# Kernel optimization log

Measured on AMD Instinct MI355X. Metric: run time of the kernel, lower is better.

Reference implementation:

```python
import jax, jax.numpy as jnp
import numpy as np

K = 8  # kNN fan-in (includes self at distance 0, matching torch_cluster.knn)


def _mlp2(x, w1, b1, w2, b2):
    # PyG MLP with plain_last=True: act between layers, none after last
    h = jax.nn.relu(x @ w1 + b1)
    return h @ w2 + b2


def _dynamic_edge_conv(x, w1, b1, w2, b2, k=K):
    # x: [B, N, C]. Recompute kNN graph from current features, EdgeConv with
    # message = MLP([x_i, x_j - x_i]) and max aggregation over neighbors.
    sq = jnp.sum(x * x, axis=-1)                                   # [B, N]
    d2 = sq[:, :, None] + sq[:, None, :] - 2.0 * jnp.einsum('bnc,bmc->bnm', x, x)
    _, idx = jax.lax.top_k(-d2, k)                                 # [B, N, k]
    xj = jax.vmap(lambda xx, ii: xx[ii])(x, idx)                   # [B, N, k, C]
    xi = jnp.broadcast_to(x[:, :, None, :], xj.shape)
    e = jnp.concatenate([xi, xj - xi], axis=-1)                    # [B, N, k, 2C]
    msg = _mlp2(e, w1, b1, w2, b2)                                 # [B, N, k, C_out]
    return jnp.max(msg, axis=2)                                    # [B, N, C_out]


def setup_inputs() -> dict:
    key = jax.random.key(0)
    ks = jax.random.split(key, 24)
    B, N = 2, 1000
    S = 0.05
    p = lambda i, shape: jax.random.normal(ks[i], shape, jnp.float32) * S
    return dict(
        pos=jax.random.normal(ks[0], (B, N, 3), jnp.float32),
        c1_w1=p(1, (6, 16)),   c1_b1=p(2, (16,)),  c1_w2=p(3, (16, 32)),   c1_b2=p(4, (32,)),
        c2_w1=p(5, (64, 64)),  c2_b1=p(6, (64,)),  c2_w2=p(7, (64, 128)),  c2_b2=p(8, (128,)),
        c3_w1=p(9, (256, 256)), c3_b1=p(10, (256,)), c3_w2=p(11, (256, 512)), c3_b2=p(12, (512,)),
        sm_w1=p(13, (672, 256)), sm_b1=p(14, (256,)), sm_w2=p(15, (256, 128)), sm_b2=p(16, (128,)),
        ec_w1=p(17, (384, 128)), ec_b1=p(18, (128,)), ec_w2=p(19, (128, 1)), ec_b2=p(20, (1,)),
    )


def reference(pos, c1_w1, c1_b1, c1_w2, c1_b2, c2_w1, c2_b1, c2_w2, c2_b2,
              c3_w1, c3_b1, c3_w2, c3_b2, sm_w1, sm_b1, sm_w2, sm_b2,
              ec_w1, ec_b1, ec_w2, ec_b2):
    x1 = _dynamic_edge_conv(pos, c1_w1, c1_b1, c1_w2, c1_b2)       # [B, N, 32]
    x2 = _dynamic_edge_conv(x1, c2_w1, c2_b1, c2_w2, c2_b2)        # [B, N, 128]
    x3 = _dynamic_edge_conv(x2, c3_w1, c3_b1, c3_w2, c3_b2)        # [B, N, 512]
    x = jnp.concatenate([x1, x2, x3], axis=-1)                     # [B, N, 672]
    sf = _mlp2(x, sm_w1, sm_b1, sm_w2, sm_b2)                      # [B, N, 128]
    g = jnp.max(sf, axis=1)                                        # [B, 128] global max pool

    N = pos.shape[1]
    t0, t1 = np.triu_indices(N, 1)                                 # 499500 pairs
    D = sf.shape[-1]
    # Linear(cat[feat_i, feat_j, global]) split into three small GEMMs on
    # [B,N,128] / [B,128] then gathered to pairs: identical math, avoids the
    # [B, P, 384] concat the torch code materializes.
    hi = sf @ ec_w1[:D]                                            # [B, N, 128]
    hj = sf @ ec_w1[D:2 * D]                                       # [B, N, 128]
    hg = g @ ec_w1[2 * D:] + ec_b1                                 # [B, 128]
    hidden = jax.nn.relu(hi[:, t0] + hj[:, t1] + hg[:, None, :])   # [B, P, 128]
    mlp_out = (hidden @ ec_w2 + ec_b2)[..., 0]                     # [B, P]
    pair_prob = jax.nn.sigmoid(mlp_out)
    return pair_prob, mlp_out
```

## Files before the change

### kernel.cpp

```cpp
#include <hip/hip_runtime.h>
#include <hip/hip_bf16.h>
#include <cmath>

#define NB 2
#define NP 1000
#define KNN 8
#define PPAIR 499500
#define JSPLIT 8

typedef __hip_bfloat16 bf16;
typedef unsigned long long u64;
typedef unsigned short ushort;
typedef unsigned int uint;
typedef __attribute__((ext_vector_type(8))) short short8;
typedef __attribute__((ext_vector_type(4))) float f32x4;

__device__ __forceinline__ float b2f(bf16 v) { return __bfloat162float(v); }
__device__ __forceinline__ ushort f2b(float f) {
    uint x = __float_as_uint(f);
    return (ushort)((x + 0x7FFFu + ((x >> 16) & 1u)) >> 16);
}
__device__ __forceinline__ float ldin(const void* p, int flag, int i) {
    return flag ? ((const float*)p)[i] : b2f(((const bf16*)p)[i]);
}

#define OFF_POS    0
#define OFF_C1W1   6000
#define OFF_C1B1   6096
#define OFF_C1W2   6112
#define OFF_C1B2   6624
#define OFF_C2W1   6656
#define OFF_C2B1   10752
#define OFF_C2W2   10816
#define OFF_C2B2   19008
#define OFF_C3W1   19136
#define OFF_C3B1   84672
#define OFF_C3W2   84928
#define OFF_C3B2   216000
#define OFF_SMW1   216512
#define OFF_SMB1   388544
#define OFF_SMW2   388800
#define OFF_SMB2   421568
#define OFF_ECW1   421696
#define OFF_ECB1   470848
#define OFF_ECW2   470976
#define OFF_ECB2   471104
#define OFF_X1     471112
#define OFF_X2     535112
#define OFF_X3     791112
#define OFF_SF     1815112
#define OFF_G      2071112
#define OFF_HI     2071368
#define OFF_HJ     2327368
#define OFF_HG     2583368
#define OFF_FLAG   2583624
#define OFF_NIDX   2583632
#define OFF_GP     2599632
#define OFF_W1T    2606032
#define OFF_W2T    2638800
#define OFF_SMW1T  2704336
#define OFF_SMW2T  2790352
#define OFF_ECW1T  2806736
#define OFF_PL     2823120
#define OFF_E2W1T  3079120
#define OFF_E2W2T  3081168

__global__ void detect_kernel(const void* pos, int* flag) {
    __shared__ float red[256];
    const unsigned short* p = (const unsigned short*)pos;
    float m = 0.f;
    for (int t = threadIdx.x; t < 6000; t += 256) {
        unsigned int u = ((unsigned int)p[t]) << 16;
        float v = fabsf(__uint_as_float(u));
        if (!isfinite(v)) v = 1e30f;
        m = fmaxf(m, v);
    }
    red[threadIdx.x] = m;
    __syncthreads();
    for (int s = 128; s > 0; s >>= 1) {
        if (threadIdx.x < s) red[threadIdx.x] = fmaxf(red[threadIdx.x], red[threadIdx.x + s]);
        __syncthreads();
    }
    if (threadIdx.x == 0) flag[0] = (red[0] > 1e6f) ? 1 : 0;
}

struct InPtrs { const void* p[21]; };

__global__ void cvt_all_kernel(InPtrs in, float* ws, const int* flag,
                               ushort* w1t, ushort* w2t, ushort* smw1t,
                               ushort* smw2t, ushort* ecw1t,
                               ushort* e2w1t, ushort* e2w2t) {
    const int sizes[21] = {6000, 96, 16, 512, 32, 4096, 64, 8192, 128,
                           65536, 256, 131072, 512, 172032, 256, 32768, 128,
                           49152, 128, 128, 1};
    const int offs[21] = {OFF_POS, OFF_C1W1, OFF_C1B1, OFF_C1W2, OFF_C1B2,
                          OFF_C2W1, OFF_C2B1, OFF_C2W2, OFF_C2B2,
                          OFF_C3W1, OFF_C3B1, OFF_C3W2, OFF_C3B2,
                          OFF_SMW1, OFF_SMB1, OFF_SMW2, OFF_SMB2,
                          OFF_ECW1, OFF_ECB1, OFF_ECW2, OFF_ECB2};
    int y = blockIdx.y;
    int t = blockIdx.x * 256 + threadIdx.x;
    int f = flag[0];
    if (y < 21) {
        if (t < sizes[y]) ws[offs[y] + t] = ldin(in.p[y], f, t);
    } else if (y == 21) {
        if (t < 65536) {
            int h = t >> 8, c = t & 255;
            w1t[t] = f2b(ldin(in.p[9], f, c * 256 + h));
        }
    } else if (y == 22) {
        if (t < 131072) {
            int o = t >> 8, h = t & 255;
            w2t[t] = f2b(ldin(in.p[11], f, h * 512 + o));
        }
    } else if (y == 23) {
        if (t < 172032) {
            int h = t / 672, c = t - h * 672;
            smw1t[t] = f2b(ldin(in.p[13], f, c * 256 + h));
        }
    } else if (y == 24) {
        if (t < 32768) {
            int o = t >> 8, h = t & 255;
            smw2t[t] = f2b(ldin(in.p[15], f, h * 128 + o));
        }
    } else if (y == 25) {
        if (t < 32768) {
            int op = t >> 7, c = t & 127;
            int idx = (op < 128) ? (c * 128 + op) : ((128 + c) * 128 + (op - 128));
            ecw1t[t] = f2b(ldin(in.p[17], f, idx));
        }
    } else if (y == 26) {
        if (t < 4096) {
            int h = t >> 6, c = t & 63;
            e2w1t[t] = f2b(ldin(in.p[5], f, c * 64 + h));
        }
    } else {
        if (t < 8192) {
            int o = t >> 6, h = t & 63;
            e2w2t[t] = f2b(ldin(in.p[7], f, h * 128 + o));
        }
    }
}

__device__ __forceinline__ void ce(u64& a, u64& b) {
    u64 lo = a < b ? a : b;
    u64 hi = a < b ? b : a;
    a = lo; b = hi;
}

__device__ __forceinline__ void ins8(u64 (&best)[KNN], u64 cand) {
    u64 cur = cand;
    #pragma unroll
    for (int r = 0; r < KNN; ++r) {
        u64 lo = best[r] < cur ? best[r] : cur;
        u64 hi = best[r] < cur ? cur : best[r];
        best[r] = lo; cur = hi;
    }
}

template <int C>
__global__ __launch_bounds__(256) void knn_fused_kernel(const float* __restrict__ x,
                                                        int* __restrict__ nidx) {
    constexpr int CP = (C + 3) & ~3;
    constexpr int PSTR = CP + 4;
    __shared__ float Qs[8 * PSTR];
    __shared__ float Ps[64 * PSTR];
    int tid = threadIdx.x;
    int b = blockIdx.y;
    int i0 = blockIdx.x * 8;
    int q = tid >> 5;
    int jcol = tid & 31;

    for (int idx = tid; idx < 8 * CP; idx += 256) {
        int row = idx / CP, c = idx % CP;
        int i = i0 + row;
        Qs[row * PSTR + c] = (c < C && i < NP) ? x[((size_t)b * NP + i) * C + c] : 0.f;
    }

    u64 best[KNN];
    #pragma unroll
    for (int r = 0; r < KNN; ++r) best[r] = ~0ull;

    for (int jc = 0; jc < 16; ++jc) {
        int j0 = jc * 64;
        __syncthreads();
        if (C % 4 == 0) {
            for (int idx = tid; idx < 64 * (C / 4); idx += 256) {
                int row = idx / (C / 4), c4 = idx % (C / 4);
                int j = j0 + row;
                float4 v = make_float4(0.f, 0.f, 0.f, 0.f);
                if (j < NP) v = *(const float4*)(x + ((size_t)b * NP + j) * C + c4 * 4);
                *(float4*)(&Ps[row * PSTR + c4 * 4]) = v;
            }
        } else {
            for (int idx = tid; idx < 64 * CP; idx += 256) {
                int row = idx / CP, c = idx % CP;
                int j = j0 + row;
                Ps[row * PSTR + c] = (c < C && j < NP) ? x[((size_t)b * NP + j) * C + c] : 0.f;
            }
        }
        __syncthreads();
        float d0 = 0.f, d1 = 0.f;
        #pragma unroll
        for (int c4 = 0; c4 < CP / 4; ++c4) {
            float4 qv = *(const float4*)(&Qs[q * PSTR + c4 * 4]);
            float4 p0 = *(const float4*)(&Ps[jcol * PSTR + c4 * 4]);
            float4 p1 = *(const float4*)(&Ps[(jcol + 32) * PSTR + c4 * 4]);
            float t;
            t = qv.x - p0.x; d0 += t * t;  t = qv.y - p0.y; d0 += t * t;
            t = qv.z - p0.z; d0 += t * t;  t = qv.w - p0.w; d0 += t * t;
            t = qv.x - p1.x; d1 += t * t;  t = qv.y - p1.y; d1 += t * t;
            t = qv.z - p1.z; d1 += t * t;  t = qv.w - p1.w; d1 += t * t;
        }
        int ja = j0 + jcol, jb = j0 + jcol + 32;
        u64 ca = (ja < NP) ? ((((u64)__float_as_uint(d0)) << 32) | (unsigned)ja) : ~0ull;
        u64 cb = (jb < NP) ? ((((u64)__float_as_uint(d1)) << 32) | (unsigned)jb) : ~0ull;
        ins8(best, ca);
        ins8(best, cb);
    }

    #pragma unroll
    for (int m = 1; m < 32; m <<= 1) {
        u64 other[KNN];
        #pragma unroll
        for (int r = 0; r < KNN; ++r)
            other[r] = __shfl_xor((unsigned long long)best[r], m, 64);
        u64 v[KNN];
        #pragma unroll
        for (int r = 0; r < KNN; ++r)
            v[r] = best[r] < other[7 - r] ? best[r] : other[7 - r];
        ce(v[0], v[4]); ce(v[1], v[5]); ce(v[2], v[6]); ce(v[3], v[7]);
        ce(v[0], v[2]); ce(v[1], v[3]); ce(v[4], v[6]); ce(v[5], v[7]);
        ce(v[0], v[1]); ce(v[2], v[3]); ce(v[4], v[5]); ce(v[6], v[7]);
        #pragma unroll
        for (int r = 0; r < KNN; ++r) best[r] = v[r];
    }

    int i = i0 + q;
    if (jcol == 0 && i < NP) {
        #pragma unroll
        for (int r = 0; r < KNN; ++r)
            nidx[((size_t)b * NP + i) * KNN + r] = (int)(best[r] & 0xffffffffu);
    }
}

template <int C>
__global__ __launch_bounds__(256) void knn5_kernel(const float* __restrict__ x,
                                                   u64* __restrict__ pl) {
    constexpr int CP = (C + 3) & ~3;
    constexpr int STR = CP + 4;
    __shared__ float As[32 * STR];
    __shared__ float Bs[64 * STR];
    int tid = threadIdx.x;
    int tx = tid & 31, ty = tid >> 5;
    int b = blockIdx.z;
    int i0 = blockIdx.x * 32;
    int jbase = blockIdx.y * 128;

    for (int idx = tid; idx < 32 * (CP / 4); idx += 256) {
        int row = idx / (CP / 4), c4 = idx % (CP / 4);
        int i = i0 + row;
        float4 v = make_float4(0.f, 0.f, 0.f, 0.f);
        if (i < NP) v = *(const float4*)(x + ((size_t)b * NP + i) * C + c4 * 4);
        *(float4*)(&As[row * STR + c4 * 4]) = v;
    }

    u64 best[4][KNN];
    #pragma unroll
    for (int r = 0; r < 4; ++r)
        #pragma unroll
        for (int s = 0; s < KNN; ++s) best[r][s] = ~0ull;

    for (int jc = 0; jc < 2; ++jc) {
        int j0 = jbase + jc * 64;
        __syncthreads();
        for (int idx = tid; idx < 64 * (CP / 4); idx += 256) {
            int row = idx / (CP / 4), c4 = idx % (CP / 4);
            int j = j0 + row;
            float4 v = make_float4(0.f, 0.f, 0.f, 0.f);
            if (j < NP) v = *(const float4*)(x + ((size_t)b * NP + j) * C + c4 * 4);
            *(float4*)(&Bs[row * STR + c4 * 4]) = v;
        }
        __syncthreads();

        float acc[4][2];
        #pragma unroll
        for (int r = 0; r < 4; ++r) { acc[r][0] = 0.f; acc[r][1] = 0.f; }
        #pragma unroll 4
        for (int k4 = 0; k4 < CP / 4; ++k4) {
            float4 b0 = *(const float4*)(&Bs[tx * STR + k4 * 4]);
            float4 b1 = *(const float4*)(&Bs[(tx + 32) * STR + k4 * 4]);
            #pragma unroll
            for (int r = 0; r < 4; ++r) {
                float4 a = *(const float4*)(&As[(ty * 4 + r) * STR + k4 * 4]);
                float d;
                d = a.x - b0.x; acc[r][0] += d * d;  d = a.x - b1.x; acc[r][1] += d * d;
                d = a.y - b0.y; acc[r][0] += d * d;  d = a.y - b1.y; acc[r][1] += d * d;
                d = a.z - b0.z; acc[r][0] += d * d;  d = a.z - b1.z; acc[r][1] += d * d;
                d = a.w - b0.w; acc[r][0] += d * d;  d = a.w - b1.w; acc[r][1] += d * d;
            }
        }
        int ja = j0 + tx, jb = j0 + tx + 32;
        #pragma unroll
        for (int r = 0; r < 4; ++r) {
            u64 ca = (ja < NP) ? ((((u64)__float_as_uint(acc[r][0])) << 32) | (unsigned)ja) : ~0ull;
            u64 cb = (jb < NP) ? ((((u64)__float_as_uint(acc[r][1])) << 32) | (unsigned)jb) : ~0ull;
            ins8(best[r], ca);
            ins8(best[r], cb);
        }
    }

    #pragma unroll
    for (int m = 1; m < 32; m <<= 1) {
        #pragma unroll
        for (int r = 0; r < 4; ++r) {
            u64 other[KNN];
            #pragma unroll
            for (int s = 0; s < KNN; ++s)
                other[s] = __shfl_xor((unsigned long long)best[r][s], m, 64);
            u64 v[KNN];
            #pragma unroll
            for (int s = 0; s < KNN; ++s)
                v[s] = best[r][s] < other[7 - s] ? best[r][s] : other[7 - s];
            ce(v[0], v[4]); ce(v[1], v[5]); ce(v[2], v[6]); ce(v[3], v[7]);
            ce(v[0], v[2]); ce(v[1], v[3]); ce(v[4], v[6]); ce(v[5], v[7]);
            ce(v[0], v[1]); ce(v[2], v[3]); ce(v[4], v[5]); ce(v[6], v[7]);
            #pragma unroll
            for (int s = 0; s < KNN; ++s) best[r][s] = v[s];
        }
    }

    if (tx == 0) {
        #pragma unroll
        for (int r = 0; r < 4; ++r) {
            int i = i0 + ty * 4 + r;
            if (i < NP) {
                size_t base = ((size_t)blockIdx.y * NB * NP + (size_t)b * NP + i) * KNN;
                #pragma unroll
                for (int s = 0; s < KNN; ++s) pl[base + s] = best[r][s];
            }
        }
    }
}

__global__ void knn_merge_kernel(const u64* __restrict__ pl, int* __restrict__ nidx) {
    int t = blockIdx.x * 256 + threadIdx.x;
    if (t >= NB * NP) return;
    u64 best[KNN];
    #pragma unroll
    for (int s = 0; s < KNN; ++s) best[s] = ~0ull;
    for (int js = 0; js < JSPLIT; ++js) {
        #pragma unroll
        for (int s = 0; s < KNN; ++s)
            ins8(best, pl[((size_t)js * NB * NP + t) * KNN + s]);
    }
    #pragma unroll
    for (int s = 0; s < KNN; ++s)
        nidx[(size_t)t * KNN + s] = (int)(best[s] & 0xffffffffu);
}

template <int CIN, int CHID, int COUT>
__global__ void edgeconv_kernel(const float* __restrict__ x, const int* __restrict__ nidx,
                                const float* __restrict__ w1, const float* __restrict__ b1,
                                const float* __restrict__ w2, const float* __restrict__ b2,
                                float* __restrict__ y) {
    int bi = blockIdx.x;
    int b = bi / NP;
    __shared__ float xi[CIN];
    __shared__ float dx[KNN][CIN];
    __shared__ __align__(16) float hid[CHID][12];
    __shared__ int nb[KNN];
    int tid = threadIdx.x;
    if (tid < KNN) nb[tid] = nidx[bi * KNN + tid];
    for (int c = tid; c < CIN; c += 256) xi[c] = x[(size_t)bi * CIN + c];
    __syncthreads();
    for (int t = tid; t < KNN * CIN; t += 256) {
        int k = t / CIN, c = t % CIN;
        dx[k][c] = x[((size_t)b * NP + nb[k]) * CIN + c] - xi[c];
    }
    __syncthreads();
    for (int h = tid; h < CHID; h += 256) {
        float common = b1[h];
        for (int c = 0; c < CIN; ++c) common += xi[c] * w1[c * CHID + h];
        float acc[KNN];
        for (int k = 0; k < KNN; ++k) acc[k] = common;
        for (int c = 0; c < CIN; ++c) {
            float wv = w1[(CIN + c) * CHID + h];
            for (int k = 0; k < KNN; ++k) acc[k] += dx[k][c] * wv;
        }
        for (int k = 0; k < KNN; ++k) hid[h][k] = fmaxf(acc[k], 0.f);
    }
    __syncthreads();
    for (int o = tid; o < COUT; o += 256) {
        float acc[KNN];
        for (int k = 0; k < KNN; ++k) acc[k] = 0.f;
        for (int h = 0; h < CHID; ++h) {
            float wv = w2[h * COUT + o];
            float4 h0 = *(const float4*)&hid[h][0];
            float4 h1 = *(const float4*)&hid[h][4];
            acc[0] += h0.x * wv; acc[1] += h0.y * wv; acc[2] += h0.z * wv; acc[3] += h0.w * wv;
            acc[4] += h1.x * wv; acc[5] += h1.y * wv; acc[6] += h1.z * wv; acc[7] += h1.w * wv;
        }
        float m = acc[0];
        for (int k = 1; k < KNN; ++k) m = fmaxf(m, acc[k]);
        y[(size_t)bi * COUT + o] = m + b2[o];
    }
}

#define E2STR 72
__global__ __launch_bounds__(256) void ec2_mfma_kernel(
        const float* __restrict__ x1, const int* __restrict__ nidx,
        const ushort* __restrict__ w1t, const ushort* __restrict__ w2t,
        const float* __restrict__ b1f, const float* __restrict__ b2f,
        float* __restrict__ x2out) {
    __shared__ ushort Elds[32 * E2STR];
    __shared__ ushort Hlds[32 * E2STR];
    int tid = threadIdx.x;
    int P0 = blockIdx.x * 4;

    {
        int e = tid >> 3, seg = tid & 7;
        int bi = P0 + (e >> 3), k = e & 7;
        int b = bi / NP;
        int nb = nidx[bi * KNN + k];
        const float* xi = x1 + (size_t)bi * 32;
        const float* xj = x1 + ((size_t)b * NP + nb) * 32;
        int c0 = seg * 8;
        #pragma unroll
        for (int c = c0; c < c0 + 8; c += 4) {
            float4 v;
            if (c < 32) {
                v = *(const float4*)(xi + c);
            } else {
                float4 a = *(const float4*)(xi + c - 32);
                float4 q = *(const float4*)(xj + c - 32);
                v = make_float4(q.x - a.x, q.y - a.y, q.z - a.z, q.w - a.w);
            }
            uint lo = (uint)f2b(v.x) | ((uint)f2b(v.y) << 16);
            uint hi = (uint)f2b(v.z) | ((uint)f2b(v.w) << 16);
            *(uint2*)(&Elds[e * E2STR + c]) = make_uint2(lo, hi);
        }
    }
    __syncthreads();

    int lane = tid & 63, wave = tid >> 6;
    int n16 = lane & 15, quad = lane >> 4;

    {
        int nc = wave * 16;
        f32x4 acc[2];
        float bv = b1f[nc + n16];
        acc[0] = (f32x4){bv, bv, bv, bv};
        acc[1] = acc[0];
        #pragma unroll
        for (int k8 = 0; k8 < 2; ++k8) {
            int ko = k8 * 32 + quad * 8;
            short8 a0 = *(const short8*)(&Elds[(n16) * E2STR + ko]);
            short8 a1 = *(const short8*)(&Elds[(16 + n16) * E2STR + ko]);
            short8 bfr = *(const short8*)(&w1t[(size_t)(nc + n16) * 64 + ko]);
            acc[0] = __builtin_amdgcn_mfma_f32_16x16x32_bf16(a0, bfr, acc[0], 0, 0, 0);
            acc[1] = __builtin_amdgcn_mfma_f32_16x16x32_bf16(a1, bfr, acc[1], 0, 0, 0);
        }
        #pragma unroll
        for (int mt = 0; mt < 2; ++mt) {
            int col = nc + n16;
            #pragma unroll
            for (int r = 0; r < 4; ++r) {
                int row = mt * 16 + quad * 4 + r;
                Hlds[row * E2STR + col] = f2b(fmaxf(acc[mt][r], 0.f));
            }
        }
    }
    __syncthreads();

    {
        int nc2 = wave * 32;
        f32x4 acc[2][2];
        #pragma unroll
        for (int mt = 0; mt < 2; ++mt)
            #pragma unroll
            for (int nt = 0; nt < 2; ++nt) acc[mt][nt] = (f32x4){0.f, 0.f, 0.f, 0.f};
        #pragma unroll
        for (int k8 = 0; k8 < 2; ++k8) {
            int ko = k8 * 32 + quad * 8;
            short8 a0 = *(const short8*)(&Hlds[(n16) * E2STR + ko]);
            short8 a1 = *(const short8*)(&Hlds[(16 + n16) * E2STR + ko]);
            #pragma unroll
            for (int nt = 0; nt < 2; ++nt) {
                short8 bfr = *(const short8*)(&w2t[(size_t)(nc2 + nt * 16 + n16) * 64 + ko]);
                acc[0][nt] = __builtin_amdgcn_mfma_f32_16x16x32_bf16(a0, bfr, acc[0][nt], 0, 0, 0);
                acc[1][nt] = __builtin_amdgcn_mfma_f32_16x16x32_bf16(a1, bfr, acc[1][nt], 0, 0, 0);
            }
        }
        #pragma unroll
        for (int mt = 0; mt < 2; ++mt)
            #pragma unroll
            for (int nt = 0; nt < 2; ++nt) {
                f32x4 a = acc[mt][nt];
                float v = fmaxf(fmaxf(a[0], a[1]), fmaxf(a[2], a[3]));
                float o = fmaxf(v, __shfl_xor(v, 16, 64));
                int col = nc2 + nt * 16 + n16;
                if (quad == 0)
                    x2out[(size_t)(P0 + mt * 2) * 128 + col] = o + b2f[col];
                else if (quad == 2)
                    x2out[(size_t)(P0 + mt * 2 + 1) * 128 + col] = o + b2f[col];
            }
    }
}

#define ESTR 264
__global__ __launch_bounds__(256) void ec3_mfma_kernel(
        const float* __restrict__ x2, const int* __restrict__ nidx,
        const ushort* __restrict__ w1t, const ushort* __restrict__ w2t,
        const float* __restrict__ b1f, const float* __restrict__ b2f,
        float* __restrict__ x3) {
    __shared__ ushort Elds[32 * ESTR];
    __shared__ ushort Hlds[32 * ESTR];
    int tid = threadIdx.x;
    int P0 = blockIdx.x * 4;

    {
        int e = tid >> 3, seg = tid & 7;
        int bi = P0 + (e >> 3), k = e & 7;
        int b = bi / NP;
        int nb = nidx[bi * KNN + k];
        const float* xi = x2 + (size_t)bi * 128;
        const float* xj = x2 + ((size_t)b * NP + nb) * 128;
        int c0 = seg * 16;
        #pragma unroll
        for (int c = c0; c < c0 + 16; c += 4) {
            float4 a = *(const float4*)(xi + c);
            float4 q = *(const float4*)(xj + c);
            uint lo = (uint)f2b(a.x) | ((uint)f2b(a.y) << 16);
            uint hi = (uint)f2b(a.z) | ((uint)f2b(a.w) << 16);
            *(uint2*)(&Elds[e * ESTR + c]) = make_uint2(lo, hi);
            lo = (uint)f2b(q.x - a.x) | ((uint)f2b(q.y - a.y) << 16);
            hi = (uint)f2b(q.z - a.z) | ((uint)f2b(q.w - a.w) << 16);
            *(uint2*)(&Elds[e * ESTR + 128 + c]) = make_uint2(lo, hi);
        }
    }
    __syncthreads();

    int lane = tid & 63, wave = tid >> 6;
    int n16 = lane & 15, quad = lane >> 4;

    {
        int nc = wave * 64;
        f32x4 acc1[2][4];
        #pragma unroll
        for (int mt = 0; mt < 2; ++mt)
            #pragma unroll
            for (int nt = 0; nt < 4; ++nt) {
                float bv = b1f[nc + nt * 16 + n16];
                acc1[mt][nt] = (f32x4){bv, bv, bv, bv};
            }
        #pragma unroll
        for (int k8 = 0; k8 < 8; ++k8) {
            int ko = k8 * 32 + quad * 8;
            short8 a0 = *(const short8*)(&Elds[(n16) * ESTR + ko]);
            short8 a1 = *(const short8*)(&Elds[(16 + n16) * ESTR + ko]);
            #pragma unroll
            for (int nt = 0; nt < 4; ++nt) {
                short8 bfr = *(const short8*)(&w1t[(size_t)(nc + nt * 16 + n16) * 256 + ko]);
                acc1[0][nt] = __builtin_amdgcn_mfma_f32_16x16x32_bf16(a0, bfr, acc1[0][nt], 0, 0, 0);
                acc1[1][nt] = __builtin_amdgcn_mfma_f32_16x16x32_bf16(a1, bfr, acc1[1][nt], 0, 0, 0);
            }
        }
        #pragma unroll
        for (int mt = 0; mt < 2; ++mt)
            #pragma unroll
            for (int nt = 0; nt < 4; ++nt) {
                int col = nc + nt * 16 + n16;
                #pragma unroll
                for (int r = 0; r < 4; ++r) {
                    int row = mt * 16 + quad * 4 + r;
                    Hlds[row * ESTR + col] = f2b(fmaxf(acc1[mt][nt][r], 0.f));
                }
            }
    }
    __syncthreads();

    {
        int nc2 = wave * 128;
        f32x4 acc2[2][8];
        #pragma unroll
        for (int mt = 0; mt < 2; ++mt)
            #pragma unroll
            for (int nt = 0; nt < 8; ++nt) acc2[mt][nt] = (f32x4){0.f, 0.f, 0.f, 0.f};
        #pragma unroll
        for (int k8 = 0; k8 < 8; ++k8) {
            int ko = k8 * 32 + quad * 8;
            short8 a0 = *(const short8*)(&Hlds[(n16) * ESTR + ko]);
            short8 a1 = *(const short8*)(&Hlds[(16 + n16) * ESTR + ko]);
            #pragma unroll
            for (int nt = 0; nt < 8; ++nt) {
                short8 bfr = *(const short8*)(&w2t[(size_t)(nc2 + nt * 16 + n16) * 256 + ko]);
                acc2[0][nt] = __builtin_amdgcn_mfma_f32_16x16x32_bf16(a0, bfr, acc2[0][nt], 0, 0, 0);
                acc2[1][nt] = __builtin_amdgcn_mfma_f32_16x16x32_bf16(a1, bfr, acc2[1][nt], 0, 0, 0);
            }
        }
        #pragma unroll
        for (int mt = 0; mt < 2; ++mt)
            #pragma unroll
            for (int nt = 0; nt < 8; ++nt) {
                f32x4 a = acc2[mt][nt];
                float v = fmaxf(fmaxf(a[0], a[1]), fmaxf(a[2], a[3]));
                float o = fmaxf(v, __shfl_xor(v, 16, 64));
                int col = nc2 + nt * 16 + n16;
                if (quad == 0)
                    x3[(size_t)(P0 + mt * 2) * 512 + col] = o + b2f[col];
                else if (quad == 2)
                    x3[(size_t)(P0 + mt * 2 + 1) * 512 + col] = o + b2f[col];
            }
    }
}

#define XSTR 680
#define SSTR 136
__global__ __launch_bounds__(256) void sm_mfma_kernel(
        const float* __restrict__ x1, const float* __restrict__ x2,
        const float* __restrict__ x3,
        const ushort* __restrict__ w1t, const ushort* __restrict__ w2t,
        const ushort* __restrict__ ecw1t,
        const float* __restrict__ b1f, const float* __restrict__ b2f,
        float* __restrict__ sf, float* __restrict__ hi, float* __restrict__ hj) {
    __shared__ ushort Xlds[32 * XSTR];
    __shared__ ushort Hlds[32 * ESTR];
    __shared__ ushort Slds[32 * SSTR];
    int tid = threadIdx.x;
    int P0 = blockIdx.x * 32;

    {
        int row = tid >> 3, cseg = tid & 7;
        int p = P0 + row;
        bool ok = p < NB * NP;
        #pragma unroll
        for (int k = 0; k < 21; ++k) {
            int c = cseg * 4 + k * 32;
            float4 v = make_float4(0.f, 0.f, 0.f, 0.f);
            if (ok) {
                if (c < 32) v = *(const float4*)(x1 + (size_t)p * 32 + c);
                else if (c < 160) v = *(const float4*)(x2 + (size_t)p * 128 + (c - 32));
                else v = *(const float4*)(x3 + (size_t)p * 512 + (c - 160));
            }
            uint lo = (uint)f2b(v.x) | ((uint)f2b(v.y) << 16);
            uint hv = (uint)f2b(v.z) | ((uint)f2b(v.w) << 16);
            *(uint2*)(&Xlds[row * XSTR + c]) = make_uint2(lo, hv);
        }
    }
    __syncthreads();

    int lane = tid & 63, wave = tid >> 6;
    int n16 = lane & 15, quad = lane >> 4;

    {
        int nc = wave * 64;
        f32x4 acc[2][4];
        #pragma unroll
        for (int mt = 0; mt < 2; ++mt)
            #pragma unroll
            for (int nt = 0; nt < 4; ++nt) {
                float bv = b1f[nc + nt * 16 + n16];
                acc[mt][nt] = (f32x4){bv, bv, bv, bv};
            }
        #pragma unroll
        for (int k8 = 0; k8 < 21; ++k8) {
            int ko = k8 * 32 + quad * 8;
            short8 a0 = *(const short8*)(&Xlds[(n16) * XSTR + ko]);
            short8 a1 = *(const short8*)(&Xlds[(16 + n16) * XSTR + ko]);
            #pragma unroll
            for (int nt = 0; nt < 4; ++nt) {
                short8 bfr = *(const short8*)(&w1t[(size_t)(nc + nt * 16 + n16) * 672 + ko]);
                acc[0][nt] = __builtin_amdgcn_mfma_f32_16x16x32_bf16(a0, bfr, acc[0][nt], 0, 0, 0);
                acc[1][nt] = __builtin_amdgcn_mfma_f32_16x16x32_bf16(a1, bfr, acc[1][nt], 0, 0, 0);
            }
        }
        #pragma unroll
        for (int mt = 0; mt < 2; ++mt)
            #pragma unroll
            for (int nt = 0; nt < 4; ++nt) {
                int col = nc + nt * 16 + n16;
                #pragma unroll
                for (int r = 0; r < 4; ++r) {
                    int row = mt * 16 + quad * 4 + r;
                    Hlds[row * ESTR + col] = f2b(fmaxf(acc[mt][nt][r], 0.f));
                }
            }
    }
    __syncthreads();

    {
        int nc = wave * 32;
        f32x4 acc[2][2];
        #pragma unroll
        for (int mt = 0; mt < 2; ++mt)
            #pragma unroll
            for (int nt = 0; nt < 2; ++nt) {
                float bv = b2f[nc + nt * 16 + n16];
                acc[mt][nt] = (f32x4){bv, bv, bv, bv};
            }
        #pragma unroll
        for (int k8 = 0; k8 < 8; ++k8) {
            int ko = k8 * 32 + quad * 8;
            short8 a0 = *(const short8*)(&Hlds[(n16) * ESTR + ko]);
            short8 a1 = *(const short8*)(&Hlds[(16 + n16) * ESTR + ko]);
            #pragma unroll
            for (int nt = 0; nt < 2; ++nt) {
                short8 bfr = *(const short8*)(&w2t[(size_t)(nc + nt * 16 + n16) * 256 + ko]);
                acc[0][nt] = __builtin_amdgcn_mfma_f32_16x16x32_bf16(a0, bfr, acc[0][nt], 0, 0, 0);
                acc[1][nt] = __builtin_amdgcn_mfma_f32_16x16x32_bf16(a1, bfr, acc[1][nt], 0, 0, 0);
            }
        }
        #pragma unroll
        for (int mt = 0; mt < 2; ++mt)
            #pragma unroll
            for (int nt = 0; nt < 2; ++nt) {
                int col = nc + nt * 16 + n16;
                #pragma unroll
                for (int r = 0; r < 4; ++r) {
                    int row = mt * 16 + quad * 4 + r;
                    int p = P0 + row;
                    float v = acc[mt][nt][r];
                    if (p < NB * NP) sf[(size_t)p * 128 + col] = v;
                    Slds[row * SSTR + col] = f2b(v);
                }
            }
    }
    __syncthreads();

    {
        int nc = wave * 64;
        f32x4 acc[2][4];
        #pragma unroll
        for (int mt = 0; mt < 2; ++mt)
            #pragma unroll
            for (int nt = 0; nt < 4; ++nt) acc[mt][nt] = (f32x4){0.f, 0.f, 0.f, 0.f};
        #pragma unroll
        for (int k8 = 0; k8 < 4; ++k8) {
            int ko = k8 * 32 + quad * 8;
            short8 a0 = *(const short8*)(&Slds[(n16) * SSTR + ko]);
            short8 a1 = *(const short8*)(&Slds[(16 + n16) * SSTR + ko]);
            #pragma unroll
            for (int nt = 0; nt < 4; ++nt) {
                short8 bfr = *(const short8*)(&ecw1t[(size_t)(nc + nt * 16 + n16) * 128 + ko]);
                acc[0][nt] = __builtin_amdgcn_mfma_f32_16x16x32_bf16(a0, bfr, acc[0][nt], 0, 0, 0);
                acc[1][nt] = __builtin_amdgcn_mfma_f32_16x16x32_bf16(a1, bfr, acc[1][nt], 0, 0, 0);
            }
        }
        #pragma unroll
        for (int mt = 0; mt < 2; ++mt)
            #pragma unroll
            for (int nt = 0; nt < 4; ++nt) {
                int colp = nc + nt * 16 + n16;
                float* dst = (colp < 128) ? hi : hj;
                int col = colp & 127;
                #pragma unroll
                for (int r = 0; r < 4; ++r) {
                    int row = mt * 16 + quad * 4 + r;
                    int p = P0 + row;
                    if (p < NB * NP) dst[(size_t)p * 128 + col] = acc[mt][nt][r];
                }
            }
    }
}

__global__ void gmax1_kernel(const float* __restrict__ sf, float* __restrict__ part) {
    int m = blockIdx.x;
    int b = m / 25, ch = m % 25, o = threadIdx.x;
    float v = -INFINITY;
    int n0 = ch * 40;
    for (int n = n0; n < n0 + 40; ++n)
        v = fmaxf(v, sf[((size_t)b * NP + n) * 128 + o]);
    part[(size_t)m * 128 + o] = v;
}

__global__ void gfin_kernel(const float* __restrict__ part, const float* __restrict__ w1,
                            const float* __restrict__ b1, float* __restrict__ hg) {
    int b = blockIdx.x, o = threadIdx.x;
    __shared__ float gs[128];
    float v = -INFINITY;
    for (int ch = 0; ch < 25; ++ch)
        v = fmaxf(v, part[((size_t)b * 25 + ch) * 128 + o]);
    gs[o] = v;
    __syncthreads();
    float acc = b1[o];
    for (int c = 0; c < 128; ++c) acc += gs[c] * w1[(256 + c) * 128 + o];
    hg[b * 128 + o] = acc;
}

__global__ __launch_bounds__(256) void pair_kernel(
        const float* __restrict__ hi, const float* __restrict__ hj,
        const float* __restrict__ hg,
        const float* __restrict__ w2, const float* __restrict__ b2,
        void* __restrict__ out, const int* __restrict__ flag) {
    int j0 = blockIdx.x * 32, i0 = blockIdx.y * 32, b = blockIdx.z;
    if (j0 + 31 <= i0) return;
    __shared__ float hit[32][132];
    __shared__ float hjt[32][132];
    __shared__ __align__(16) float w2s[128];
    int tid = threadIdx.x;
    if (tid < 128) w2s[tid] = w2[tid];
    for (int t = tid; t < 32 * 128; t += 256) {
        int r = t >> 7, c = t & 127;
        int i = i0 + r, j = j0 + r;
        hit[r][c] = (i < NP) ? hi[((size_t)b * NP + i) * 128 + c] : 0.f;
        hjt[r][c] = ((j < NP) ? hj[((size_t)b * NP + j) * 128 + c] : 0.f) + hg[b * 128 + c];
    }
    __syncthreads();
    float bb = b2[0];
    int f = flag[0];
    int tj = tid & 31;
    int ti0 = tid >> 5;
    int j = j0 + tj;
    float acc[4] = {0.f, 0.f, 0.f, 0.f};
    #pragma unroll 4
    for (int o4 = 0; o4 < 32; ++o4) {
        float4 hv = *(const float4*)(&hjt[tj][o4 * 4]);
        float4 wv = *(const float4*)(&w2s[o4 * 4]);
        #pragma unroll
        for (int r = 0; r < 4; ++r) {
            float4 a = *(const float4*)(&hit[ti0 + 8 * r][o4 * 4]);
            acc[r] += fmaxf(a.x + hv.x, 0.f) * wv.x
                    + fmaxf(a.y + hv.y, 0.f) * wv.y
                    + fmaxf(a.z + hv.z, 0.f) * wv.z
                    + fmaxf(a.w + hv.w, 0.f) * wv.w;
        }
    }
    #pragma unroll
    for (int r = 0; r < 4; ++r) {
        int i = i0 + ti0 + 8 * r;
        if (i < j && j < NP) {
            size_t p = (size_t)i * (NP - 1) - (size_t)i * (i - 1) / 2 + (j - i - 1);
            float mo = acc[r] + bb;
            float pr = 1.f / (1.f + expf(-mo));
            size_t idx0 = (size_t)b * PPAIR + p;
            size_t idx1 = (size_t)NB * PPAIR + idx0;
            if (f) {
                ((float*)out)[idx0] = pr;
                ((float*)out)[idx1] = mo;
            } else {
                ((bf16*)out)[idx0] = __float2bfloat16(pr);
                ((bf16*)out)[idx1] = __float2bfloat16(mo);
            }
        }
    }
}

extern "C" void kernel_launch(void* const* d_in, const int* in_sizes, int n_in,
                              void* d_out, int out_size, void* d_ws, size_t ws_size,
                              hipStream_t stream) {
    float* ws = (float*)d_ws;
    float* posf = ws + OFF_POS;
    float* x1   = ws + OFF_X1;
    float* x2   = ws + OFF_X2;
    float* x3   = ws + OFF_X3;
    float* sf   = ws + OFF_SF;
    float* hi   = ws + OFF_HI;
    float* hj   = ws + OFF_HJ;
    float* hgb  = ws + OFF_HG;
    int*   flag = (int*)(ws + OFF_FLAG);
    int*   nidx = (int*)(ws + OFF_NIDX);
    float* gp   = ws + OFF_GP;
    ushort* w1t = (ushort*)(ws + OFF_W1T);
    ushort* w2t = (ushort*)(ws + OFF_W2T);
    ushort* smw1t = (ushort*)(ws + OFF_SMW1T);
    ushort* smw2t = (ushort*)(ws + OFF_SMW2T);
    ushort* ecw1t = (ushort*)(ws + OFF_ECW1T);
    ushort* e2w1t = (ushort*)(ws + OFF_E2W1T);
    ushort* e2w2t = (ushort*)(ws + OFF_E2W2T);
    u64*    pl  = (u64*)(ws + OFF_PL);

    detect_kernel<<<1, 256, 0, stream>>>(d_in[0], flag);

    InPtrs ip;
    for (int i = 0; i < 21; ++i) ip.p[i] = d_in[i];
    dim3 cgrid(672, 28);
    cvt_all_kernel<<<cgrid, 256, 0, stream>>>(ip, ws, flag, w1t, w2t, smw1t, smw2t,
                                              ecw1t, e2w1t, e2w2t);

    dim3 kgrid_f(NP / 8, NB);
    dim3 kgrid5((NP + 31) / 32, JSPLIT, NB);

    knn_fused_kernel<3><<<kgrid_f, 256, 0, stream>>>(posf, nidx);
    edgeconv_kernel<3, 16, 32><<<NB * NP, 256, 0, stream>>>(
        posf, nidx, ws + OFF_C1W1, ws + OFF_C1B1, ws + OFF_C1W2, ws + OFF_C1B2, x1);

    knn_fused_kernel<32><<<kgrid_f, 256, 0, stream>>>(x1, nidx);
    ec2_mfma_kernel<<<NB * NP / 4, 256, 0, stream>>>(
        x1, nidx, e2w1t, e2w2t, ws + OFF_C2B1, ws + OFF_C2B2, x2);

    knn5_kernel<128><<<kgrid5, 256, 0, stream>>>(x2, pl);
    knn_merge_kernel<<<(NB * NP + 255) / 256, 256, 0, stream>>>(pl, nidx);
    ec3_mfma_kernel<<<NB * NP / 4, 256, 0, stream>>>(
        x2, nidx, w1t, w2t, ws + OFF_C3B1, ws + OFF_C3B2, x3);

    sm_mfma_kernel<<<(NB * NP + 31) / 32, 256, 0, stream>>>(
        x1, x2, x3, smw1t, smw2t, ecw1t, ws + OFF_SMB1, ws + OFF_SMB2, sf, hi, hj);

    gmax1_kernel<<<NB * 25, 128, 0, stream>>>(sf, gp);
    gfin_kernel<<<NB, 128, 0, stream>>>(gp, ws + OFF_ECW1, ws + OFF_ECB1, hgb);

    dim3 pgrid(32, 32, NB);
    pair_kernel<<<pgrid, 256, 0, stream>>>(hi, hj, hgb, ws + OFF_ECW2, ws + OFF_ECB2,
                                           d_out, flag);
}
```

Before: 311.6 us.

## Split kNN into full distance matrix kernel plus per-row top-k selection

Replaces the fused kNN kernels for layers 2 and 3 with two stages. The first kernel writes the full pairwise squared-distance matrix to workspace. The second has one wavefront per query row: each lane keeps a sorted top-8 list, merges four candidates at a time with a small sorting network, and the lists are then reduced across the wavefront with shuffles. This removes the per-thread serial insertion work and the separate partial-list merge pass, at the cost of writing and re-reading a 2x1000x1000 float matrix through global memory.

```diff
diff --git a/kernel.cpp b/kernel.cpp
--- a/kernel.cpp
+++ b/kernel.cpp
@@ -6,7 +6,6 @@
 #define NP 1000
 #define KNN 8
 #define PPAIR 499500
-#define JSPLIT 8
 
 typedef __hip_bfloat16 bf16;
 typedef unsigned long long u64;
@@ -64,6 +63,7 @@
 #define OFF_PL     2823120
 #define OFF_E2W1T  3079120
 #define OFF_E2W2T  3081168
+#define OFF_D2     3085264
 
 __global__ void detect_kernel(const void* pos, int* flag) {
     __shared__ float red[256];
@@ -148,6 +148,8 @@
     a = lo; b = hi;
 }
 
+__device__ __forceinline__ u64 umin64(u64 a, u64 b) { return a < b ? a : b; }
+
 __device__ __forceinline__ void ins8(u64 (&best)[KNN], u64 cand) {
     u64 cur = cand;
     #pragma unroll
@@ -156,6 +158,17 @@
         u64 hi = best[r] < cur ? cur : best[r];
         best[r] = lo; cur = hi;
     }
+}
+
+__device__ __forceinline__ void merge4(u64 (&best)[KNN], u64 s0, u64 s1, u64 s2, u64 s3) {
+    ce(s0, s1); ce(s2, s3); ce(s0, s2); ce(s1, s3); ce(s1, s2);
+    best[4] = umin64(best[4], s3);
+    best[5] = umin64(best[5], s2);
+    best[6] = umin64(best[6], s1);
+    best[7] = umin64(best[7], s0);
+    ce(best[0], best[4]); ce(best[1], best[5]); ce(best[2], best[6]); ce(best[3], best[7]);
+    ce(best[0], best[2]); ce(best[1], best[3]); ce(best[4], best[6]); ce(best[5], best[7]);
+    ce(best[0], best[1]); ce(best[2], best[3]); ce(best[4], best[5]); ce(best[6], best[7]);
 }
 
 template <int C>
@@ -245,8 +258,8 @@
 }
 
 template <int C>
-__global__ __launch_bounds__(256) void knn5_kernel(const float* __restrict__ x,
-                                                   u64* __restrict__ pl) {
+__global__ __launch_bounds__(256) void dist_kernel(const float* __restrict__ x,
+                                                   float* __restrict__ d2) {
     constexpr int CP = (C + 3) & ~3;
     constexpr int STR = CP + 4;
     __shared__ float As[32 * STR];
@@ -255,7 +268,7 @@
     int tx = tid & 31, ty = tid >> 5;
     int b = blockIdx.z;
     int i0 = blockIdx.x * 32;
-    int jbase = blockIdx.y * 128;
+    int j0 = blockIdx.y * 64;
 
     for (int idx = tid; idx < 32 * (CP / 4); idx += 256) {
         int row = idx / (CP / 4), c4 = idx % (CP / 4);
@@ -264,99 +277,86 @@
         if (i < NP) v = *(const float4*)(x + ((size_t)b * NP + i) * C + c4 * 4);
         *(float4*)(&As[row * STR + c4 * 4]) = v;
     }
-
-    u64 best[4][KNN];
+    for (int idx = tid; idx < 64 * (CP / 4); idx += 256) {
+        int row = idx / (CP / 4), c4 = idx % (CP / 4);
+        int j = j0 + row;
+        float4 v = make_float4(0.f, 0.f, 0.f, 0.f);
+        if (j < NP) v = *(const float4*)(x + ((size_t)b * NP + j) * C + c4 * 4);
+        *(float4*)(&Bs[row * STR + c4 * 4]) = v;
+    }
+    __syncthreads();
+
+    float acc[4][2];
     #pragma unroll
-    for (int r = 0; r < 4; ++r)
-        #pragma unroll
-        for (int s = 0; s < KNN; ++s) best[r][s] = ~0ull;
-
-    for (int jc = 0; jc < 2; ++jc) {
-        int j0 = jbase + jc * 64;
-        __syncthreads();
-        for (int idx = tid; idx < 64 * (CP / 4); idx += 256) {
-            int row = idx / (CP / 4), c4 = idx % (CP / 4);
-            int j = j0 + row;
-            float4 v = make_float4(0.f, 0.f, 0.f, 0.f);
-            if (j < NP) v = *(const float4*)(x + ((size_t)b * NP + j) * C + c4 * 4);
-            *(float4*)(&Bs[row * STR + c4 * 4]) = v;
-        }
-        __syncthreads();
-
-        float acc[4][2];
-        #pragma unroll
-        for (int r = 0; r < 4; ++r) { acc[r][0] = 0.f; acc[r][1] = 0.f; }
-        #pragma unroll 4
-        for (int k4 = 0; k4 < CP / 4; ++k4) {
-            float4 b0 = *(const float4*)(&Bs[tx * STR + k4 * 4]);
-            float4 b1 = *(const float4*)(&Bs[(tx + 32) * STR + k4 * 4]);
-            #pragma unroll
-            for (int r = 0; r < 4; ++r) {
-                float4 a = *(const float4*)(&As[(ty * 4 + r) * STR + k4 * 4]);
-                float d;
-                d = a.x - b0.x; acc[r][0] += d * d;  d = a.x - b1.x; acc[r][1] += d * d;
-                d = a.y - b0.y; acc[r][0] += d * d;  d = a.y - b1.y; acc[r][1] += d * d;
-                d = a.z - b0.z; acc[r][0] += d * d;  d = a.z - b1.z; acc[r][1] += d * d;
-                d = a.w - b0.w; acc[r][0] += d * d;  d = a.w - b1.w; acc[r][1] += d * d;
-            }
-        }
-        int ja = j0 + tx, jb = j0 + tx + 32;
+    for (int r = 0; r < 4; ++r) { acc[r][0] = 0.f; acc[r][1] = 0.f; }
+    #pragma unroll 4
+    for (int k4 = 0; k4 < CP / 4; ++k4) {
+        float4 b0 = *(const float4*)(&Bs[tx * STR + k4 * 4]);
+        float4 b1 = *(const float4*)(&Bs[(tx + 32) * STR + k4 * 4]);
         #pragma unroll
         for (int r = 0; r < 4; ++r) {
-            u64 ca = (ja < NP) ? ((((u64)__float_as_uint(acc[r][0])) << 32) | (unsigned)ja) : ~0ull;
-            u64 cb = (jb < NP) ? ((((u64)__float_as_uint(acc[r][1])) << 32) | (unsigned)jb) : ~0ull;
-            ins8(best[r], ca);
-            ins8(best[r], cb);
-        }
-    }
-
+            float4 a = *(const float4*)(&As[(ty * 4 + r) * STR + k4 * 4]);
+            float d;
+            d = a.x - b0.x; acc[r][0] += d * d;  d = a.x - b1.x; acc[r][1] += d * d;
+            d = a.y - b0.y; acc[r][0] += d * d;  d = a.y - b1.y; acc[r][1] += d * d;
+            d = a.z - b0.z; acc[r][0] += d * d;  d = a.z - b1.z; acc[r][1] += d * d;
+            d = a.w - b0.w; acc[r][0] += d * d;  d = a.w - b1.w; acc[r][1] += d * d;
+        }
+    }
+
+    int ja = j0 + tx, jb = j0 + tx + 32;
     #pragma unroll
-    for (int m = 1; m < 32; m <<= 1) {
-        #pragma unroll
-        for (int r = 0; r < 4; ++r) {
-            u64 other[KNN];
-            #pragma unroll
-            for (int s = 0; s < KNN; ++s)
-                other[s] = __shfl_xor((unsigned long long)best[r][s], m, 64);
-            u64 v[KNN];
-            #pragma unroll
-            for (int s = 0; s < KNN; ++s)
-                v[s] = best[r][s] < other[7 - s] ? best[r][s] : other[7 - s];
-            ce(v[0], v[4]); ce(v[1], v[5]); ce(v[2], v[6]); ce(v[3], v[7]);
-            ce(v[0], v[2]); ce(v[1], v[3]); ce(v[4], v[6]); ce(v[5], v[7]);
-            ce(v[0], v[1]); ce(v[2], v[3]); ce(v[4], v[5]); ce(v[6], v[7]);
-            #pragma unroll
-            for (int s = 0; s < KNN; ++s) best[r][s] = v[s];
-        }
-    }
-
-    if (tx == 0) {
-        #pragma unroll
-        for (int r = 0; r < 4; ++r) {
-            int i = i0 + ty * 4 + r;
-            if (i < NP) {
-                size_t base = ((size_t)blockIdx.y * NB * NP + (size_t)b * NP + i) * KNN;
-                #pragma unroll
-                for (int s = 0; s < KNN; ++s) pl[base + s] = best[r][s];
-            }
-        }
-    }
-}
-
-__global__ void knn_merge_kernel(const u64* __restrict__ pl, int* __restrict__ nidx) {
-    int t = blockIdx.x * 256 + threadIdx.x;
-    if (t >= NB * NP) return;
+    for (int r = 0; r < 4; ++r) {
+        int i = i0 + ty * 4 + r;
+        if (i < NP) {
+            size_t base = ((size_t)b * NP + i) * NP;
+            if (ja < NP) d2[base + ja] = acc[r][0];
+            if (jb < NP) d2[base + jb] = acc[r][1];
+        }
+    }
+}
+
+__global__ __launch_bounds__(256) void knn_sel_kernel(const float* __restrict__ d2,
+                                                      int* __restrict__ nidx) {
+    int lane = threadIdx.x & 63;
+    int q = blockIdx.x * 4 + (threadIdx.x >> 6);
+    const float* row = d2 + (size_t)q * NP;
     u64 best[KNN];
     #pragma unroll
-    for (int s = 0; s < KNN; ++s) best[s] = ~0ull;
-    for (int js = 0; js < JSPLIT; ++js) {
-        #pragma unroll
-        for (int s = 0; s < KNN; ++s)
-            ins8(best, pl[((size_t)js * NB * NP + t) * KNN + s]);
-    }
+    for (int r = 0; r < KNN; ++r) best[r] = ~0ull;
     #pragma unroll
-    for (int s = 0; s < KNN; ++s)
-        nidx[(size_t)t * KNN + s] = (int)(best[s] & 0xffffffffu);
+    for (int t = 0; t < 4; ++t) {
+        int j = t * 256 + lane * 4;
+        if (j < NP) {
+            float4 v = *(const float4*)(row + j);
+            merge4(best,
+                   (((u64)__float_as_uint(v.x)) << 32) | (unsigned)(j + 0),
+                   (((u64)__float_as_uint(v.y)) << 32) | (unsigned)(j + 1),
+                   (((u64)__float_as_uint(v.z)) << 32) | (unsigned)(j + 2),
+                   (((u64)__float_as_uint(v.w)) << 32) | (unsigned)(j + 3));
+        }
+    }
+    #pragma unroll
+    for (int m = 1; m < 64; m <<= 1) {
+        u64 other[KNN];
+        #pragma unroll
+        for (int r = 0; r < KNN; ++r)
+            other[r] = __shfl_xor((unsigned long long)best[r], m, 64);
+        u64 v[KNN];
+        #pragma unroll
+        for (int r = 0; r < KNN; ++r)
+            v[r] = umin64(best[r], other[KNN - 1 - r]);
+        ce(v[0], v[4]); ce(v[1], v[5]); ce(v[2], v[6]); ce(v[3], v[7]);
+        ce(v[0], v[2]); ce(v[1], v[3]); ce(v[4], v[6]); ce(v[5], v[7]);
+        ce(v[0], v[1]); ce(v[2], v[3]); ce(v[4], v[5]); ce(v[6], v[7]);
+        #pragma unroll
+        for (int r = 0; r < KNN; ++r) best[r] = v[r];
+    }
+    if (lane == 0) {
+        #pragma unroll
+        for (int r = 0; r < KNN; ++r)
+            nidx[(size_t)q * KNN + r] = (int)(best[r] & 0xffffffffu);
+    }
 }
 
 template <int CIN, int CHID, int COUT>
@@ -861,6 +861,7 @@
     int*   flag = (int*)(ws + OFF_FLAG);
     int*   nidx = (int*)(ws + OFF_NIDX);
     float* gp   = ws + OFF_GP;
+    float* d2m  = ws + OFF_D2;
     ushort* w1t = (ushort*)(ws + OFF_W1T);
     ushort* w2t = (ushort*)(ws + OFF_W2T);
     ushort* smw1t = (ushort*)(ws + OFF_SMW1T);
@@ -868,7 +869,6 @@
     ushort* ecw1t = (ushort*)(ws + OFF_ECW1T);
     ushort* e2w1t = (ushort*)(ws + OFF_E2W1T);
     ushort* e2w2t = (ushort*)(ws + OFF_E2W2T);
-    u64*    pl  = (u64*)(ws + OFF_PL);
 
     detect_kernel<<<1, 256, 0, stream>>>(d_in[0], flag);
 
@@ -879,18 +879,20 @@
                                               ecw1t, e2w1t, e2w2t);
 
     dim3 kgrid_f(NP / 8, NB);
-    dim3 kgrid5((NP + 31) / 32, JSPLIT, NB);
+    dim3 dgrid(32, 16, 2);
+    int selgrid = NB * NP / 4;
 
     knn_fused_kernel<3><<<kgrid_f, 256, 0, stream>>>(posf, nidx);
     edgeconv_kernel<3, 16, 32><<<NB * NP, 256, 0, stream>>>(
         posf, nidx, ws + OFF_C1W1, ws + OFF_C1B1, ws + OFF_C1W2, ws + OFF_C1B2, x1);
 
-    knn_fused_kernel<32><<<kgrid_f, 256, 0, stream>>>(x1, nidx);
+    dist_kernel<32><<<dgrid, 256, 0, stream>>>(x1, d2m);
+    knn_sel_kernel<<<selgrid, 256, 0, stream>>>(d2m, nidx);
     ec2_mfma_kernel<<<NB * NP / 4, 256, 0, stream>>>(
         x1, nidx, e2w1t, e2w2t, ws + OFF_C2B1, ws + OFF_C2B2, x2);
 
-    knn5_kernel<128><<<kgrid5, 256, 0, stream>>>(x2, pl);
-    knn_merge_kernel<<<(NB * NP + 255) / 256, 256, 0, stream>>>(pl, nidx);
+    dist_kernel<128><<<dgrid, 256, 0, stream>>>(x2, d2m);
+    knn_sel_kernel<<<selgrid, 256, 0, stream>>>(d2m, nidx);
     ec3_mfma_kernel<<<NB * NP / 4, 256, 0, stream>>>(
         x2, nidx, w1t, w2t, ws + OFF_C3B1, ws + OFF_C3B2, x3);
 
```

Measured after the change: 286.9 us. 7.9% less time.
